# Kernel optimization log

Measured on AMD Instinct MI355X. Metric: run time of the kernel, lower is better.

## Reference

```python
import jax, jax.numpy as jnp
import numpy as np

FT = 0.2  # clip floor (init arg ft)

def _norm_mat(m):
    # matrix / (count of nonzeros along last dim + 1e-30)
    deg = jnp.sum(m != 0, axis=-1, keepdims=True).astype(m.dtype)
    return m / (deg + 1e-30)

def _l2n(x):
    return x / (jnp.linalg.norm(x, axis=-1, keepdims=True) + 1e-30)

def setup_inputs():
    B, L, D, H, O = 2, 2048, 64, 64, 128
    N = 2 * L
    ks = jax.random.split(jax.random.key(0), 30)
    u = lambda i, s: jax.random.uniform(ks[i], s, jnp.float32)
    g = lambda i, s: jax.random.normal(ks[i], s, jnp.float32) * 0.05
    inp = {}
    inp['word_outputs_0'] = g(0, (B, L, D))
    inp['word_outputs_1'] = g(1, (B, L, D))
    inp['node_hidden'] = g(2, (B, D))
    inp['op_embedding'] = g(3, (B, O, D))
    inp['word_exist_sequence'] = (u(4, (B, N)) < 0.8).astype(jnp.float32)
    inp['word_exist_matrix'] = (u(5, (B, N, N)) < 0.8).astype(jnp.float32)
    inp['word_operator'] = (u(6, (B, N, O)) < 0.02).astype(jnp.float32)
    inp['word_word'] = (u(7, (B, N, N)) < 0.01).astype(jnp.float32)
    inp['depend_0'] = (u(8, (B, L, L)) < 0.05).astype(jnp.float32)
    inp['depend_1'] = (u(9, (B, L, L)) < 0.05).astype(jnp.float32)
    inp['goal_word'] = u(10, (B, N))
    names = [('Wg', (D, H)), ('bg', (H,)), ('Wwk', (D, H)), ('bwk', (H,)),
             ('Wws', (D, H)), ('bws', (H,)), ('Wo', (D, D)), ('bo', (D,)),
             ('Wupd', (3 * H, D)), ('bupd', (D,)), ('Wf', (3 * H + D, D)), ('bf', (D,)),
             ('Wf2', (2 * D, D)), ('bf2', (D,)), ('Wout', (D, D)), ('bout', (D,))]
    for i, (nm, s) in enumerate(names):
        inp[nm] = g(11 + i, s)
    return inp

def _forward(w0, w1, nh, opE, wes, wem, wop, ww, d0, d1, gw,
             Wg, bg, Wwk, bwk, Wws, bws, Wo, bo, Wupd, bupd, Wf, bf, Wf2, bf2, Wout, bout):
    all_w = jnp.concatenate([w0, w1], axis=1)                      # [B,N,D]
    goal_trans = (nh @ Wg + bg)[:, None, :]                        # [B,1,H] (broadcast = expand)
    word_g = _l2n(goal_trans * gw[..., None])                      # [B,N,H]
    word_w_k = _l2n(jnp.matmul(_norm_mat(ww * wem), all_w @ Wwk + bwk))
    ws0 = jnp.matmul(_norm_mat(d0), w0 @ Wws + bws)
    ws1 = jnp.matmul(_norm_mat(d1), w1 @ Wws + bws)
    word_w_s = _l2n(jnp.concatenate([ws0, ws1], axis=1))           # [B,N,H]
    neigh = jnp.concatenate([word_g, word_w_k, word_w_s], axis=-1)  # [B,N,3H]
    forget = jax.nn.sigmoid(jnp.concatenate([all_w, word_g, word_w_k, word_w_s], axis=-1) @ Wf + bf)
    word_updated = jnp.maximum(forget, FT) * all_w + (1.0 - forget) * jax.nn.relu(neigh @ Wupd + bupd)
    adj_op = _norm_mat(jnp.swapaxes(wes[..., None] * wop, 1, 2))   # [B,O,N]
    word_op = jnp.matmul(adj_op, word_updated @ Wo + bo)           # [B,O,D]
    forget2 = jax.nn.sigmoid(jnp.concatenate([opE, word_op], axis=-1) @ Wf2 + bf2)
    op_out = jnp.maximum(forget2, FT) * opE + (1.0 - forget2) * jax.nn.relu(word_op @ Wout + bout)
    # original returns (split(word_updated), op_embedding); concat along node axis here
    return jnp.concatenate([word_updated, op_out], axis=1)         # [B,N+O,D]

def reference(word_outputs_0, word_outputs_1, node_hidden, op_embedding,
              word_exist_sequence, word_exist_matrix, word_operator, word_word,
              depend_0, depend_1, goal_word,
              Wg, bg, Wwk, bwk, Wws, bws, Wo, bo, Wupd, bupd, Wf, bf, Wf2, bf2, Wout, bout):
    return _forward(word_outputs_0, word_outputs_1, node_hidden, op_embedding,
                    word_exist_sequence, word_exist_matrix, word_operator, word_word,
                    depend_0, depend_1, goal_word,
                    Wg, bg, Wwk, bwk, Wws, bws, Wo, bo, Wupd, bupd, Wf, bf, Wf2, bf2, Wout, bout)
```

## Files before the change

kernel.cpp:

```cpp
#include <hip/hip_runtime.h>
#include <cstdint>

typedef unsigned short u16;
typedef unsigned long long u64;

__device__ __forceinline__ u16 f2b(float f){
  union { float f; uint32_t i; } v; v.f = f;
  uint32_t r = v.i + 0x7FFFu + ((v.i >> 16) & 1u);
  return (u16)(r >> 16);
}
__device__ __forceinline__ float b2f(u16 u){
  union { uint32_t i; float f; } v; v.i = ((uint32_t)u) << 16; return v.f;
}
__device__ __forceinline__ float sigmoidf(float x){ return 1.0f / (1.0f + __expf(-x)); }

__device__ __forceinline__ void gl_lds16(const void* g, void* l){
  __builtin_amdgcn_global_load_lds((const __attribute__((address_space(1))) void*)g,
                                   (__attribute__((address_space(3))) void*)l, 16, 0, 0);
}
__device__ __forceinline__ void gl_lds4(const void* g, void* l){
  __builtin_amdgcn_global_load_lds((const __attribute__((address_space(1))) void*)g,
                                   (__attribute__((address_space(3))) void*)l, 4, 0, 0);
}
#define WAIT_VM0() __builtin_amdgcn_s_waitcnt(0x0F70)

__global__ void k_pre(const float* __restrict__ nh, const float* __restrict__ Wg,
                      const float* __restrict__ bg, float* __restrict__ ghat){
  int b = threadIdx.x >> 6, h = threadIdx.x & 63;
  float g = bg[h];
  for (int d = 0; d < 64; ++d) g += nh[b*64 + d] * Wg[d*64 + h];
  float ss = g * g;
  #pragma unroll
  for (int o = 32; o > 0; o >>= 1) ss += __shfl_xor(ss, o, 64);
  ghat[b*64 + h] = g / (sqrtf(ss) + 1e-30f);
}

__global__ __launch_bounds__(256) void k_xform(
    const float* __restrict__ w0, const float* __restrict__ w1,
    const float* __restrict__ Wwk, const float* __restrict__ bwk,
    const float* __restrict__ Wws, const float* __restrict__ bws,
    float* __restrict__ Xk, float* __restrict__ Xs){
  __shared__ float sWk[4096], sWs[4096];
  int tid = threadIdx.x;
  for (int i = tid; i < 1024; i += 256){
    ((float4*)sWk)[i] = ((const float4*)Wwk)[i];
    ((float4*)sWs)[i] = ((const float4*)Wws)[i];
  }
  __syncthreads();
  int lane = tid & 63, wave = tid >> 6;
  float bk = bwk[lane], bs = bws[lane];
  float aw[4];
  #pragma unroll
  for (int t = 0; t < 4; ++t){
    int row = blockIdx.x*4 + wave + t*2048;
    int b = row >> 12, n = row & 4095;
    aw[t] = (n < 2048) ? w0[((size_t)(b*2048 + n))*64 + lane]
                       : w1[((size_t)(b*2048 + n - 2048))*64 + lane];
  }
  #pragma unroll
  for (int t = 0; t < 4; ++t){
    int row = blockIdx.x*4 + wave + t*2048;
    float xk = bk, xs = bs;
    #pragma unroll 8
    for (int d = 0; d < 64; ++d){
      float a = __shfl(aw[t], d, 64);
      xk += a * sWk[d*64 + lane];
      xs += a * sWs[d*64 + lane];
    }
    Xk[(size_t)row*64 + lane] = xk;
    Xs[(size_t)row*64 + lane] = xs;
  }
}

__global__ __launch_bounds__(256) void k_bits_all(
    const float* __restrict__ ww, const float* __restrict__ wem,
    const float* __restrict__ d0, const float* __restrict__ d1,
    u64* __restrict__ bitBig, u64* __restrict__ bitD0, u64* __restrict__ bitD1){
  __shared__ float lA[4][1024];
  __shared__ float lB[4][1024];
  int wave = threadIdx.x >> 6, lane = threadIdx.x & 63;
  int wid = blockIdx.x*4 + wave;
  const float *A, *B; u64* dst; bool two;
  if (wid < 32768){
    A = ww + (size_t)wid*1024; B = wem + (size_t)wid*1024;
    dst = bitBig + (size_t)wid*16; two = true;
  } else if (wid < 40960){
    size_t c = wid - 32768; A = d0 + c*1024; B = A; dst = bitD0 + c*16; two = false;
  } else {
    size_t c = wid - 40960; A = d1 + c*1024; B = A; dst = bitD1 + c*16; two = false;
  }
  #pragma unroll
  for (int i = 0; i < 4; ++i)
    gl_lds16(A + i*256 + lane*4, &lA[wave][i*256]);
  if (two){
    #pragma unroll
    for (int i = 0; i < 4; ++i)
      gl_lds16(B + i*256 + lane*4, &lB[wave][i*256]);
  }
  WAIT_VM0();
  const float4* a4 = (const float4*)lA[wave];
  const float4* b4 = (const float4*)lB[wave];
  float4 a0 = a4[lane], a1 = a4[64 + lane], a2 = a4[128 + lane], a3 = a4[192 + lane];
  float4 b0 = two ? b4[lane] : a0, b1 = two ? b4[64 + lane] : a1;
  float4 b2 = two ? b4[128 + lane] : a2, b3 = two ? b4[192 + lane] : a3;
  u64 myw = 0;
#define B4(i, va, vb) { \
  u64 m0 = __ballot((va.x != 0.f) && (vb.x != 0.f)); \
  u64 m1 = __ballot((va.y != 0.f) && (vb.y != 0.f)); \
  u64 m2 = __ballot((va.z != 0.f) && (vb.z != 0.f)); \
  u64 m3 = __ballot((va.w != 0.f) && (vb.w != 0.f)); \
  if (lane == (i)*4 + 0) myw = m0; \
  if (lane == (i)*4 + 1) myw = m1; \
  if (lane == (i)*4 + 2) myw = m2; \
  if (lane == (i)*4 + 3) myw = m3; }
  B4(0, a0, b0) B4(1, a1, b1) B4(2, a2, b2) B4(3, a3, b3)
#undef B4
  if (lane < 16) dst[lane] = myw;
}

__global__ __launch_bounds__(64) void k_bitsop(
    const float* __restrict__ wes, const float* __restrict__ wop, u64* __restrict__ bitOp){
  int lane = threadIdx.x;
  int ng = blockIdx.x;
  float2 v = ((const float2*)(wop + (size_t)ng*128))[lane];
  float e = wes[ng];
  u64 m0 = __ballot((e != 0.f) && (v.x != 0.f));
  u64 m1 = __ballot((e != 0.f) && (v.y != 0.f));
  if (lane == 0) bitOp[(size_t)ng*2]     = m0;
  if (lane == 1) bitOp[(size_t)ng*2 + 1] = m1;
}

__global__ __launch_bounds__(256) void k_gath_all(
    const u64* __restrict__ bitBig, const u64* __restrict__ bitD0, const u64* __restrict__ bitD1,
    const float* __restrict__ Xk, const float* __restrict__ Xs,
    u16* __restrict__ wwkn, u16* __restrict__ wwsn){
  __shared__ int q[4][256];
  __shared__ float rows[4][16][64];
  int lane = threadIdx.x & 63, wave = threadIdx.x >> 6;
  int wid = blockIdx.x*4 + wave;
  const u64* bits; const float* XbBase; u16* op; int WPR;
  if (wid < 8192){
    WPR = 64; bits = bitBig + (size_t)wid*64;
    int b = wid >> 12;
    XbBase = Xk + (size_t)b*4096*64;
    op = wwkn + (size_t)wid*64;
  } else if (wid < 12288){
    int lr = wid - 8192; WPR = 32; bits = bitD0 + (size_t)lr*32;
    int b = lr >> 11, r = lr & 2047;
    XbBase = Xs + (size_t)b*4096*64;
    op = wwsn + ((size_t)b*4096 + r)*64;
  } else {
    int lr = wid - 12288; WPR = 32; bits = bitD1 + (size_t)lr*32;
    int b = lr >> 11, r = lr & 2047;
    XbBase = Xs + ((size_t)b*4096 + 2048)*64;
    op = wwsn + ((size_t)b*4096 + 2048 + r)*64;
  }
  u64 word = (lane < WPR) ? bits[lane] : 0ULL;
  int c = __popcll(word);
  int pre = c;
  #pragma unroll
  for (int off = 1; off < 64; off <<= 1){
    int t = __shfl_up(pre, off, 64);
    if (lane >= off) pre += t;
  }
  int total = __shfl(pre, 63, 64);
  int base = pre - c;
  int colhi = (lane >> 2) * 256 + (lane & 3);
  u64 m = word;
  while (m){
    int p = __builtin_ctzll(m); m &= m - 1;
    q[wave][base++] = colhi + p*4;
  }
  float acc = 0.f;
  int i = 0;
  for (; i + 16 <= total; i += 16){
    int4 c0 = *(const int4*)&q[wave][i];
    int4 c1 = *(const int4*)&q[wave][i + 4];
    int4 c2 = *(const int4*)&q[wave][i + 8];
    int4 c3 = *(const int4*)&q[wave][i + 12];
    gl_lds4(XbBase + (size_t)c0.x*64 + lane, &rows[wave][ 0][0]);
    gl_lds4(XbBase + (size_t)c0.y*64 + lane, &rows[wave][ 1][0]);
    gl_lds4(XbBase + (size_t)c0.z*64 + lane, &rows[wave][ 2][0]);
    gl_lds4(XbBase + (size_t)c0.w*64 + lane, &rows[wave][ 3][0]);
    gl_lds4(XbBase + (size_t)c1.x*64 + lane, &rows[wave][ 4][0]);
    gl_lds4(XbBase + (size_t)c1.y*64 + lane, &rows[wave][ 5][0]);
    gl_lds4(XbBase + (size_t)c1.z*64 + lane, &rows[wave][ 6][0]);
    gl_lds4(XbBase + (size_t)c1.w*64 + lane, &rows[wave][ 7][0]);
    gl_lds4(XbBase + (size_t)c2.x*64 + lane, &rows[wave][ 8][0]);
    gl_lds4(XbBase + (size_t)c2.y*64 + lane, &rows[wave][ 9][0]);
    gl_lds4(XbBase + (size_t)c2.z*64 + lane, &rows[wave][10][0]);
    gl_lds4(XbBase + (size_t)c2.w*64 + lane, &rows[wave][11][0]);
    gl_lds4(XbBase + (size_t)c3.x*64 + lane, &rows[wave][12][0]);
    gl_lds4(XbBase + (size_t)c3.y*64 + lane, &rows[wave][13][0]);
    gl_lds4(XbBase + (size_t)c3.z*64 + lane, &rows[wave][14][0]);
    gl_lds4(XbBase + (size_t)c3.w*64 + lane, &rows[wave][15][0]);
    WAIT_VM0();
    float s0 = 0.f, s1 = 0.f, s2 = 0.f, s3 = 0.f;
    #pragma unroll
    for (int r = 0; r < 4; ++r){
      s0 += rows[wave][r][lane];
      s1 += rows[wave][4 + r][lane];
      s2 += rows[wave][8 + r][lane];
      s3 += rows[wave][12 + r][lane];
    }
    acc += (s0 + s1) + (s2 + s3);
  }
  for (; i < total; ++i) acc += XbBase[(size_t)q[wave][i]*64 + lane];
  float ss = acc * acc;
  #pragma unroll
  for (int o = 32; o > 0; o >>= 1) ss += __shfl_xor(ss, o, 64);
  op[lane] = f2b(acc / (sqrtf(ss) + 1e-30f));
}

__global__ __launch_bounds__(256, 2) void k_update(
    const float* __restrict__ w0, const float* __restrict__ w1,
    const float* __restrict__ gw, const float* __restrict__ ghat,
    const u16* __restrict__ wwkn, const u16* __restrict__ wwsn,
    const float* __restrict__ Wf, const float* __restrict__ bf,
    const float* __restrict__ Wupd, const float* __restrict__ bupd,
    const float* __restrict__ Wo, const float* __restrict__ bo,
    float* __restrict__ out, float* __restrict__ WUo){
  __shared__ uint32_t pWf[8192];
  __shared__ uint32_t pWu[6144];
  __shared__ uint32_t pWo[2048];
  __shared__ float xsh[4][256];
  int tid = threadIdx.x;
  for (int i = tid; i < 8192; i += 256){
    int k2 = i >> 6, ln = i & 63;
    pWf[i] = (uint32_t)f2b(Wf[(2*k2)*64 + ln]) | ((uint32_t)f2b(Wf[(2*k2+1)*64 + ln]) << 16);
  }
  for (int i = tid; i < 6144; i += 256){
    int k2 = i >> 6, ln = i & 63;
    pWu[i] = (uint32_t)f2b(Wupd[(2*k2)*64 + ln]) | ((uint32_t)f2b(Wupd[(2*k2+1)*64 + ln]) << 16);
  }
  for (int i = tid; i < 2048; i += 256){
    int k2 = i >> 6, ln = i & 63;
    pWo[i] = (uint32_t)f2b(Wo[(2*k2)*64 + ln]) | ((uint32_t)f2b(Wo[(2*k2+1)*64 + ln]) << 16);
  }
  __syncthreads();
  int lane = tid & 63, wave = tid >> 6;
  float bff = bf[lane], bup = bupd[lane], boo = bo[lane];
  float aw[4], wgv[4], wk[4], wsv[4];
  #pragma unroll
  for (int t = 0; t < 4; ++t){
    int row = blockIdx.x*4 + wave + t*2048;
    int b = row >> 12, n = row & 4095;
    aw[t] = (n < 2048) ? w0[((size_t)(b*2048 + n))*64 + lane]
                       : w1[((size_t)(b*2048 + n - 2048))*64 + lane];
    float gvv = gw[b*4096 + n];
    wgv[t] = (gvv != 0.f) ? ghat[b*64 + lane] : 0.f;
    wk[t]  = b2f(wwkn[(size_t)row*64 + lane]);
    wsv[t] = b2f(wwsn[(size_t)row*64 + lane]);
  }
  #pragma unroll
  for (int t = 0; t < 4; ++t){
    int row = blockIdx.x*4 + wave + t*2048;
    int b = row >> 12, n = row & 4095;
    xsh[wave][lane] = aw[t]; xsh[wave][64 + lane] = wgv[t];
    xsh[wave][128 + lane] = wk[t]; xsh[wave][192 + lane] = wsv[t];
    float f = bff, u = bup;
    #pragma unroll 8
    for (int k2 = 0; k2 < 32; ++k2){
      float2 xv = *(const float2*)&xsh[wave][2*k2];
      uint32_t wf = pWf[k2*64 + lane];
      f += xv.x * b2f((u16)wf) + xv.y * b2f((u16)(wf >> 16));
    }
    #pragma unroll 8
    for (int k2 = 32; k2 < 128; ++k2){
      float2 xv = *(const float2*)&xsh[wave][2*k2];
      uint32_t wf = pWf[k2*64 + lane];
      uint32_t wu = pWu[(k2 - 32)*64 + lane];
      f += xv.x * b2f((u16)wf) + xv.y * b2f((u16)(wf >> 16));
      u += xv.x * b2f((u16)wu) + xv.y * b2f((u16)(wu >> 16));
    }
    f = sigmoidf(f);
    u = fmaxf(u, 0.f);
    float wu = fmaxf(f, 0.2f) * aw[t] + (1.f - f) * u;
    out[((size_t)b*4224 + n)*64 + lane] = wu;
    float o = boo;
    #pragma unroll 8
    for (int k2 = 0; k2 < 32; ++k2){
      uint32_t wo2 = pWo[k2*64 + lane];
      o += __shfl(wu, 2*k2, 64) * b2f((u16)wo2) + __shfl(wu, 2*k2 + 1, 64) * b2f((u16)(wo2 >> 16));
    }
    WUo[(size_t)row*64 + lane] = o;
  }
}

__global__ __launch_bounds__(256) void k_opagg(
    const u64* __restrict__ bitOp, const float* __restrict__ WUo,
    float* __restrict__ wordop){
  __shared__ int q[4][96];
  __shared__ float sacc[4][64];
  __shared__ int scnt[4];
  int tid = threadIdx.x, lane = tid & 63, wave = tid >> 6;
  int rowIdx = blockIdx.x;
  int b = rowIdx >> 7, o = rowIdx & 127;
  int wrd = o & 1, bit = o >> 1;
  const u64* bp = bitOp + (size_t)b*8192 + (size_t)wave*2048 + wrd;
  u64 lt = (1ULL << lane) - 1ULL;
  u64 vv[16];
  #pragma unroll
  for (int it = 0; it < 16; ++it) vv[it] = bp[(size_t)(it*64 + lane)*2];
  int cnt = 0;
  #pragma unroll
  for (int it = 0; it < 16; ++it){
    bool nz = (vv[it] >> bit) & 1ULL;
    u64 m = __ballot(nz);
    if (nz) q[wave][cnt + (int)__popcll(m & lt)] = wave*1024 + it*64 + lane;
    cnt += (int)__popcll(m);
  }
  const float* Xb = WUo + (size_t)b*4096*64 + lane;
  float acc = 0.f;
  int i = 0;
  for (; i + 8 <= cnt; i += 8){
    int4 c0 = *(const int4*)&q[wave][i];
    int4 c1 = *(const int4*)&q[wave][i + 4];
    float v0 = Xb[(size_t)c0.x*64], v1 = Xb[(size_t)c0.y*64];
    float v2 = Xb[(size_t)c0.z*64], v3 = Xb[(size_t)c0.w*64];
    float v4 = Xb[(size_t)c1.x*64], v5 = Xb[(size_t)c1.y*64];
    float v6 = Xb[(size_t)c1.z*64], v7 = Xb[(size_t)c1.w*64];
    acc += ((v0 + v1) + (v2 + v3)) + ((v4 + v5) + (v6 + v7));
  }
  for (; i < cnt; ++i) acc += Xb[(size_t)q[wave][i]*64];
  sacc[wave][lane] = acc;
  if (lane == 0) scnt[wave] = cnt;
  __syncthreads();
  if (wave == 0){
    float t = sacc[0][lane] + sacc[1][lane] + sacc[2][lane] + sacc[3][lane];
    float deg = (float)(scnt[0] + scnt[1] + scnt[2] + scnt[3]);
    wordop[(size_t)rowIdx*64 + lane] = t / (deg + 1e-30f);
  }
}

__global__ __launch_bounds__(256) void k_opout(
    const float* __restrict__ opE, const float* __restrict__ wordop,
    const float* __restrict__ Wf2, const float* __restrict__ bf2,
    const float* __restrict__ Wout, const float* __restrict__ bout,
    float* __restrict__ out){
  __shared__ float sW2[8192];
  __shared__ float sWo[4096];
  __shared__ float xsh[4][128];
  int tid = threadIdx.x;
  for (int i = tid; i < 2048; i += 256) ((float4*)sW2)[i] = ((const float4*)Wf2)[i];
  for (int i = tid; i < 1024; i += 256) ((float4*)sWo)[i] = ((const float4*)Wout)[i];
  __syncthreads();
  int lane = tid & 63, wave = tid >> 6;
  int row = blockIdx.x*4 + wave;
  int b = row >> 7, o = row & 127;
  float e  = opE[(size_t)row*64 + lane];
  float wo = wordop[(size_t)row*64 + lane];
  xsh[wave][lane] = e; xsh[wave][64 + lane] = wo;
  float f = bf2[lane], u = bout[lane];
  #pragma unroll 8
  for (int k = 0; k < 128; ++k) f += xsh[wave][k] * sW2[k*64 + lane];
  #pragma unroll 8
  for (int d = 0; d < 64; ++d)  u += xsh[wave][64 + d] * sWo[d*64 + lane];
  f = sigmoidf(f);
  u = fmaxf(u, 0.f);
  float res = fmaxf(f, 0.2f) * e + (1.f - f) * u;
  out[((size_t)b*4224 + 4096 + o)*64 + lane] = res;
}

extern "C" void kernel_launch(void* const* d_in, const int* in_sizes, int n_in,
                              void* d_out, int out_size, void* d_ws, size_t ws_size,
                              hipStream_t stream){
  const float* w0   = (const float*)d_in[0];
  const float* w1   = (const float*)d_in[1];
  const float* nh   = (const float*)d_in[2];
  const float* opE  = (const float*)d_in[3];
  const float* wes  = (const float*)d_in[4];
  const float* wem  = (const float*)d_in[5];
  const float* wop  = (const float*)d_in[6];
  const float* ww   = (const float*)d_in[7];
  const float* d0   = (const float*)d_in[8];
  const float* d1   = (const float*)d_in[9];
  const float* gw   = (const float*)d_in[10];
  const float* Wg   = (const float*)d_in[11];
  const float* bg   = (const float*)d_in[12];
  const float* Wwk  = (const float*)d_in[13];
  const float* bwk  = (const float*)d_in[14];
  const float* Wws  = (const float*)d_in[15];
  const float* bws  = (const float*)d_in[16];
  const float* Wo   = (const float*)d_in[17];
  const float* bo   = (const float*)d_in[18];
  const float* Wupd = (const float*)d_in[19];
  const float* bupd = (const float*)d_in[20];
  const float* Wf   = (const float*)d_in[21];
  const float* bf   = (const float*)d_in[22];
  const float* Wf2  = (const float*)d_in[23];
  const float* bf2  = (const float*)d_in[24];
  const float* Wout = (const float*)d_in[25];
  const float* bout = (const float*)d_in[26];

  float* ws   = (float*)d_ws;
  float* ghat = ws;
  float* Xk   = ws + 128;
  float* Xs   = ws + 524416;
  float* wopm = ws + 1048704;
  u64*  bitBig= (u64*)(ws + 1065088);
  u64*  bitD0 = (u64*)(ws + 2113664);
  u64*  bitD1 = (u64*)(ws + 2375808);
  u64*  bitOp = (u64*)(ws + 2637952);
  u16*  wwkn  = (u16*)(ws + 2670720);
  u16*  wwsn  = (u16*)(ws + 2932864);
  float* WUo  = Xs;
  float* out  = (float*)d_out;

  k_pre<<<1, 128, 0, stream>>>(nh, Wg, bg, ghat);
  k_xform<<<512, 256, 0, stream>>>(w0, w1, Wwk, bwk, Wws, bws, Xk, Xs);
  k_bits_all<<<12288, 256, 0, stream>>>(ww, wem, d0, d1, bitBig, bitD0, bitD1);
  k_bitsop<<<8192, 64, 0, stream>>>(wes, wop, bitOp);
  k_gath_all<<<4096, 256, 0, stream>>>(bitBig, bitD0, bitD1, Xk, Xs, wwkn, wwsn);
  k_update<<<512, 256, 0, stream>>>(w0, w1, gw, ghat, wwkn, wwsn, Wf, bf, Wupd, bupd, Wo, bo, out, WUo);
  k_opagg<<<256, 256, 0, stream>>>(bitOp, WUo, wopm);
  k_opout<<<64, 256, 0, stream>>>(opE, wopm, Wf2, bf2, Wout, bout, out);
}
```

Baseline: 463.6 us.

## Merge small kernels, pre-pack bf16 weights once, and load bit masks directly

Folds the goal-vector kernel and the bf16 weight packing into extra blocks of k_xform, so k_update just copies pre-packed weights into shared memory instead of re-converting them in every block. The operator bitmask pass is merged into k_bits_all as extra waves. The operator aggregation and output kernels are fused into one kernel. k_bits_all now loads directly into registers instead of going through global-to-LDS loads. The aim is to cut launch count and repeated per-block conversion work. The cost is a changed bitOp word/bit indexing and heavier blocks in the fused kernels.

```diff
diff --git a/kernel.cpp b/kernel.cpp
--- a/kernel.cpp
+++ b/kernel.cpp
@@ -14,34 +14,48 @@
 }
 __device__ __forceinline__ float sigmoidf(float x){ return 1.0f / (1.0f + __expf(-x)); }
 
-__device__ __forceinline__ void gl_lds16(const void* g, void* l){
-  __builtin_amdgcn_global_load_lds((const __attribute__((address_space(1))) void*)g,
-                                   (__attribute__((address_space(3))) void*)l, 16, 0, 0);
-}
 __device__ __forceinline__ void gl_lds4(const void* g, void* l){
   __builtin_amdgcn_global_load_lds((const __attribute__((address_space(1))) void*)g,
                                    (__attribute__((address_space(3))) void*)l, 4, 0, 0);
 }
 #define WAIT_VM0() __builtin_amdgcn_s_waitcnt(0x0F70)
-
-__global__ void k_pre(const float* __restrict__ nh, const float* __restrict__ Wg,
-                      const float* __restrict__ bg, float* __restrict__ ghat){
-  int b = threadIdx.x >> 6, h = threadIdx.x & 63;
-  float g = bg[h];
-  for (int d = 0; d < 64; ++d) g += nh[b*64 + d] * Wg[d*64 + h];
-  float ss = g * g;
-  #pragma unroll
-  for (int o = 32; o > 0; o >>= 1) ss += __shfl_xor(ss, o, 64);
-  ghat[b*64 + h] = g / (sqrtf(ss) + 1e-30f);
-}
 
 __global__ __launch_bounds__(256) void k_xform(
     const float* __restrict__ w0, const float* __restrict__ w1,
     const float* __restrict__ Wwk, const float* __restrict__ bwk,
     const float* __restrict__ Wws, const float* __restrict__ bws,
-    float* __restrict__ Xk, float* __restrict__ Xs){
+    const float* __restrict__ nh, const float* __restrict__ Wg, const float* __restrict__ bg,
+    const float* __restrict__ Wf, const float* __restrict__ Wupd, const float* __restrict__ Wo,
+    float* __restrict__ Xk, float* __restrict__ Xs,
+    float* __restrict__ ghat, uint32_t* __restrict__ pkWf,
+    uint32_t* __restrict__ pkWu, uint32_t* __restrict__ pkWo){
+  int tid = threadIdx.x;
+  if (blockIdx.x >= 512){
+    int aux = blockIdx.x - 512;
+    if (aux == 16){
+      if (tid < 128){
+        int b = tid >> 6, h = tid & 63;
+        float g = bg[h];
+        for (int d = 0; d < 64; ++d) g += nh[b*64 + d] * Wg[d*64 + h];
+        float ss = g * g;
+        #pragma unroll
+        for (int o = 32; o > 0; o >>= 1) ss += __shfl_xor(ss, o, 64);
+        ghat[b*64 + h] = g / (sqrtf(ss) + 1e-30f);
+      }
+      return;
+    }
+    for (int k = tid; k < 1024; k += 256){
+      int i = aux*1024 + k;
+      const float* src; uint32_t* dst; int li;
+      if (i < 8192){ src = Wf; dst = pkWf; li = i; }
+      else if (i < 14336){ src = Wupd; dst = pkWu; li = i - 8192; }
+      else { src = Wo; dst = pkWo; li = i - 14336; }
+      int k2 = li >> 6, ln = li & 63;
+      dst[li] = (uint32_t)f2b(src[(2*k2)*64 + ln]) | ((uint32_t)f2b(src[(2*k2+1)*64 + ln]) << 16);
+    }
+    return;
+  }
   __shared__ float sWk[4096], sWs[4096];
-  int tid = threadIdx.x;
   for (int i = tid; i < 1024; i += 256){
     ((float4*)sWk)[i] = ((const float4*)Wwk)[i];
     ((float4*)sWs)[i] = ((const float4*)Wws)[i];
@@ -75,34 +89,38 @@
 __global__ __launch_bounds__(256) void k_bits_all(
     const float* __restrict__ ww, const float* __restrict__ wem,
     const float* __restrict__ d0, const float* __restrict__ d1,
-    u64* __restrict__ bitBig, u64* __restrict__ bitD0, u64* __restrict__ bitD1){
-  __shared__ float lA[4][1024];
-  __shared__ float lB[4][1024];
-  int wave = threadIdx.x >> 6, lane = threadIdx.x & 63;
-  int wid = blockIdx.x*4 + wave;
-  const float *A, *B; u64* dst; bool two;
+    const float* __restrict__ wes, const float* __restrict__ wop,
+    u64* __restrict__ bitBig, u64* __restrict__ bitD0, u64* __restrict__ bitD1,
+    u64* __restrict__ bitOp){
+  int wid = blockIdx.x*4 + (threadIdx.x >> 6);
+  int lane = threadIdx.x & 63;
+  if (wid >= 49152){
+    int ng0 = (wid - 49152) * 8;
+    #pragma unroll
+    for (int i = 0; i < 8; ++i){
+      int n = ng0 + i;
+      float vx = wop[(size_t)n*128 + lane];
+      float vy = wop[(size_t)n*128 + 64 + lane];
+      float e  = wes[n];
+      u64 m0 = __ballot((e != 0.f) && (vx != 0.f));
+      u64 m1 = __ballot((e != 0.f) && (vy != 0.f));
+      if (lane == 0) bitOp[(size_t)n*2]     = m0;
+      if (lane == 1) bitOp[(size_t)n*2 + 1] = m1;
+    }
+    return;
+  }
+  const float *A, *B; u64* dst;
   if (wid < 32768){
-    A = ww + (size_t)wid*1024; B = wem + (size_t)wid*1024;
-    dst = bitBig + (size_t)wid*16; two = true;
+    A = ww + (size_t)wid*1024; B = wem + (size_t)wid*1024; dst = bitBig + (size_t)wid*16;
   } else if (wid < 40960){
-    size_t c = wid - 32768; A = d0 + c*1024; B = A; dst = bitD0 + c*16; two = false;
+    size_t c = wid - 32768; A = d0 + c*1024; B = A; dst = bitD0 + c*16;
   } else {
-    size_t c = wid - 40960; A = d1 + c*1024; B = A; dst = bitD1 + c*16; two = false;
-  }
-  #pragma unroll
-  for (int i = 0; i < 4; ++i)
-    gl_lds16(A + i*256 + lane*4, &lA[wave][i*256]);
-  if (two){
-    #pragma unroll
-    for (int i = 0; i < 4; ++i)
-      gl_lds16(B + i*256 + lane*4, &lB[wave][i*256]);
-  }
-  WAIT_VM0();
-  const float4* a4 = (const float4*)lA[wave];
-  const float4* b4 = (const float4*)lB[wave];
-  float4 a0 = a4[lane], a1 = a4[64 + lane], a2 = a4[128 + lane], a3 = a4[192 + lane];
-  float4 b0 = two ? b4[lane] : a0, b1 = two ? b4[64 + lane] : a1;
-  float4 b2 = two ? b4[128 + lane] : a2, b3 = two ? b4[192 + lane] : a3;
+    size_t c = wid - 40960; A = d1 + c*1024; B = A; dst = bitD1 + c*16;
+  }
+  const float4* ap = (const float4*)A + lane;
+  const float4* bp = (const float4*)B + lane;
+  float4 a0 = ap[0], a1 = ap[64], a2 = ap[128], a3 = ap[192];
+  float4 b0 = bp[0], b1 = bp[64], b2 = bp[128], b3 = bp[192];
   u64 myw = 0;
 #define B4(i, va, vb) { \
   u64 m0 = __ballot((va.x != 0.f) && (vb.x != 0.f)); \
@@ -116,18 +134,6 @@
   B4(0, a0, b0) B4(1, a1, b1) B4(2, a2, b2) B4(3, a3, b3)
 #undef B4
   if (lane < 16) dst[lane] = myw;
-}
-
-__global__ __launch_bounds__(64) void k_bitsop(
-    const float* __restrict__ wes, const float* __restrict__ wop, u64* __restrict__ bitOp){
-  int lane = threadIdx.x;
-  int ng = blockIdx.x;
-  float2 v = ((const float2*)(wop + (size_t)ng*128))[lane];
-  float e = wes[ng];
-  u64 m0 = __ballot((e != 0.f) && (v.x != 0.f));
-  u64 m1 = __ballot((e != 0.f) && (v.y != 0.f));
-  if (lane == 0) bitOp[(size_t)ng*2]     = m0;
-  if (lane == 1) bitOp[(size_t)ng*2 + 1] = m1;
 }
 
 __global__ __launch_bounds__(256) void k_gath_all(
@@ -216,27 +222,18 @@
     const float* __restrict__ w0, const float* __restrict__ w1,
     const float* __restrict__ gw, const float* __restrict__ ghat,
     const u16* __restrict__ wwkn, const u16* __restrict__ wwsn,
-    const float* __restrict__ Wf, const float* __restrict__ bf,
-    const float* __restrict__ Wupd, const float* __restrict__ bupd,
-    const float* __restrict__ Wo, const float* __restrict__ bo,
+    const uint32_t* __restrict__ pkWf, const uint32_t* __restrict__ pkWu,
+    const uint32_t* __restrict__ pkWo,
+    const float* __restrict__ bf, const float* __restrict__ bupd, const float* __restrict__ bo,
     float* __restrict__ out, float* __restrict__ WUo){
   __shared__ uint32_t pWf[8192];
   __shared__ uint32_t pWu[6144];
   __shared__ uint32_t pWo[2048];
   __shared__ float xsh[4][256];
   int tid = threadIdx.x;
-  for (int i = tid; i < 8192; i += 256){
-    int k2 = i >> 6, ln = i & 63;
-    pWf[i] = (uint32_t)f2b(Wf[(2*k2)*64 + ln]) | ((uint32_t)f2b(Wf[(2*k2+1)*64 + ln]) << 16);
-  }
-  for (int i = tid; i < 6144; i += 256){
-    int k2 = i >> 6, ln = i & 63;
-    pWu[i] = (uint32_t)f2b(Wupd[(2*k2)*64 + ln]) | ((uint32_t)f2b(Wupd[(2*k2+1)*64 + ln]) << 16);
-  }
-  for (int i = tid; i < 2048; i += 256){
-    int k2 = i >> 6, ln = i & 63;
-    pWo[i] = (uint32_t)f2b(Wo[(2*k2)*64 + ln]) | ((uint32_t)f2b(Wo[(2*k2+1)*64 + ln]) << 16);
-  }
+  for (int i = tid; i < 2048; i += 256) ((uint4*)pWf)[i] = ((const uint4*)pkWf)[i];
+  for (int i = tid; i < 1536; i += 256) ((uint4*)pWu)[i] = ((const uint4*)pkWu)[i];
+  for (int i = tid; i < 512;  i += 256) ((uint4*)pWo)[i] = ((const uint4*)pkWo)[i];
   __syncthreads();
   int lane = tid & 63, wave = tid >> 6;
   float bff = bf[lane], bup = bupd[lane], boo = bo[lane];
@@ -287,16 +284,24 @@
   }
 }
 
-__global__ __launch_bounds__(256) void k_opagg(
+__global__ __launch_bounds__(256) void k_opfin(
     const u64* __restrict__ bitOp, const float* __restrict__ WUo,
-    float* __restrict__ wordop){
+    const float* __restrict__ opE,
+    const float* __restrict__ Wf2, const float* __restrict__ bf2,
+    const float* __restrict__ Wout, const float* __restrict__ bout,
+    float* __restrict__ out){
+  __shared__ float sW2[8192];
+  __shared__ float sWo[4096];
   __shared__ int q[4][96];
   __shared__ float sacc[4][64];
   __shared__ int scnt[4];
+  __shared__ float xsh[128];
   int tid = threadIdx.x, lane = tid & 63, wave = tid >> 6;
+  for (int i = tid; i < 2048; i += 256) ((float4*)sW2)[i] = ((const float4*)Wf2)[i];
+  for (int i = tid; i < 1024; i += 256) ((float4*)sWo)[i] = ((const float4*)Wout)[i];
   int rowIdx = blockIdx.x;
   int b = rowIdx >> 7, o = rowIdx & 127;
-  int wrd = o & 1, bit = o >> 1;
+  int wrd = o >> 6, bit = o & 63;
   const u64* bp = bitOp + (size_t)b*8192 + (size_t)wave*2048 + wrd;
   u64 lt = (1ULL << lane) - 1ULL;
   u64 vv[16];
@@ -329,37 +334,19 @@
   if (wave == 0){
     float t = sacc[0][lane] + sacc[1][lane] + sacc[2][lane] + sacc[3][lane];
     float deg = (float)(scnt[0] + scnt[1] + scnt[2] + scnt[3]);
-    wordop[(size_t)rowIdx*64 + lane] = t / (deg + 1e-30f);
-  }
-}
-
-__global__ __launch_bounds__(256) void k_opout(
-    const float* __restrict__ opE, const float* __restrict__ wordop,
-    const float* __restrict__ Wf2, const float* __restrict__ bf2,
-    const float* __restrict__ Wout, const float* __restrict__ bout,
-    float* __restrict__ out){
-  __shared__ float sW2[8192];
-  __shared__ float sWo[4096];
-  __shared__ float xsh[4][128];
-  int tid = threadIdx.x;
-  for (int i = tid; i < 2048; i += 256) ((float4*)sW2)[i] = ((const float4*)Wf2)[i];
-  for (int i = tid; i < 1024; i += 256) ((float4*)sWo)[i] = ((const float4*)Wout)[i];
-  __syncthreads();
-  int lane = tid & 63, wave = tid >> 6;
-  int row = blockIdx.x*4 + wave;
-  int b = row >> 7, o = row & 127;
-  float e  = opE[(size_t)row*64 + lane];
-  float wo = wordop[(size_t)row*64 + lane];
-  xsh[wave][lane] = e; xsh[wave][64 + lane] = wo;
-  float f = bf2[lane], u = bout[lane];
-  #pragma unroll 8
-  for (int k = 0; k < 128; ++k) f += xsh[wave][k] * sW2[k*64 + lane];
-  #pragma unroll 8
-  for (int d = 0; d < 64; ++d)  u += xsh[wave][64 + d] * sWo[d*64 + lane];
-  f = sigmoidf(f);
-  u = fmaxf(u, 0.f);
-  float res = fmaxf(f, 0.2f) * e + (1.f - f) * u;
-  out[((size_t)b*4224 + 4096 + o)*64 + lane] = res;
+    float wo = t / (deg + 1e-30f);
+    float e  = opE[(size_t)rowIdx*64 + lane];
+    xsh[lane] = e; xsh[64 + lane] = wo;
+    float f = bf2[lane], u = bout[lane];
+    #pragma unroll 8
+    for (int k = 0; k < 128; ++k) f += xsh[k] * sW2[k*64 + lane];
+    #pragma unroll 8
+    for (int d = 0; d < 64; ++d)  u += xsh[64 + d] * sWo[d*64 + lane];
+    f = sigmoidf(f);
+    u = fmaxf(u, 0.f);
+    float res = fmaxf(f, 0.2f) * e + (1.f - f) * u;
+    out[((size_t)b*4224 + 4096 + o)*64 + lane] = res;
+  }
 }
 
 extern "C" void kernel_launch(void* const* d_in, const int* in_sizes, int n_in,
@@ -393,26 +380,28 @@
   const float* Wout = (const float*)d_in[25];
   const float* bout = (const float*)d_in[26];
 
-  float* ws   = (float*)d_ws;
-  float* ghat = ws;
-  float* Xk   = ws + 128;
-  float* Xs   = ws + 524416;
-  float* wopm = ws + 1048704;
-  u64*  bitBig= (u64*)(ws + 1065088);
-  u64*  bitD0 = (u64*)(ws + 2113664);
-  u64*  bitD1 = (u64*)(ws + 2375808);
-  u64*  bitOp = (u64*)(ws + 2637952);
-  u16*  wwkn  = (u16*)(ws + 2670720);
-  u16*  wwsn  = (u16*)(ws + 2932864);
-  float* WUo  = Xs;
-  float* out  = (float*)d_out;
-
-  k_pre<<<1, 128, 0, stream>>>(nh, Wg, bg, ghat);
-  k_xform<<<512, 256, 0, stream>>>(w0, w1, Wwk, bwk, Wws, bws, Xk, Xs);
-  k_bits_all<<<12288, 256, 0, stream>>>(ww, wem, d0, d1, bitBig, bitD0, bitD1);
-  k_bitsop<<<8192, 64, 0, stream>>>(wes, wop, bitOp);
+  float* ws    = (float*)d_ws;
+  float* ghat  = ws;
+  float* Xk    = ws + 128;
+  float* Xs    = ws + 524416;
+  uint32_t* pkWf = (uint32_t*)(ws + 1048704);
+  uint32_t* pkWu = (uint32_t*)(ws + 1056896);
+  uint32_t* pkWo = (uint32_t*)(ws + 1063040);
+  u64*  bitBig = (u64*)(ws + 1065088);
+  u64*  bitD0  = (u64*)(ws + 2113664);
+  u64*  bitD1  = (u64*)(ws + 2375808);
+  u64*  bitOp  = (u64*)(ws + 2637952);
+  u16*  wwkn   = (u16*)(ws + 2670720);
+  u16*  wwsn   = (u16*)(ws + 2932864);
+  float* WUo   = Xs;
+  float* out   = (float*)d_out;
+
+  k_xform<<<529, 256, 0, stream>>>(w0, w1, Wwk, bwk, Wws, bws, nh, Wg, bg,
+                                   Wf, Wupd, Wo, Xk, Xs, ghat, pkWf, pkWu, pkWo);
+  k_bits_all<<<12544, 256, 0, stream>>>(ww, wem, d0, d1, wes, wop,
+                                        bitBig, bitD0, bitD1, bitOp);
   k_gath_all<<<4096, 256, 0, stream>>>(bitBig, bitD0, bitD1, Xk, Xs, wwkn, wwsn);
-  k_update<<<512, 256, 0, stream>>>(w0, w1, gw, ghat, wwkn, wwsn, Wf, bf, Wupd, bupd, Wo, bo, out, WUo);
-  k_opagg<<<256, 256, 0, stream>>>(bitOp, WUo, wopm);
-  k_opout<<<64, 256, 0, stream>>>(opE, wopm, Wf2, bf2, Wout, bout, out);
-}
+  k_update<<<512, 256, 0, stream>>>(w0, w1, gw, ghat, wwkn, wwsn,
+                                    pkWf, pkWu, pkWo, bf, bupd, bo, out, WUo);
+  k_opfin<<<256, 256, 0, stream>>>(bitOp, WUo, opE, Wf2, bf2, Wout, bout, out);
+}
```

Result: faster. 447.5 us (-3.5%).
